# Performance work log

Measured on AMD Instinct MI355X. Metric: run time of the kernel, lower is better.

Reference implementation:

```python
import jax, jax.numpy as jnp
import numpy as np

N_NODES = 100000
N_EDGES = 1250000
IN_CH = 128
OUT_CH = 64


def setup_inputs() -> dict:
    key = jax.random.key(0)
    k1, k2, k3, k4 = jax.random.split(key, 4)
    x = jax.random.normal(k1, (N_NODES, IN_CH), dtype=jnp.float32)
    edge_index = jax.random.randint(k2, (2, N_EDGES), 0, N_NODES, dtype=jnp.int64)
    edge_weight = jax.random.uniform(k3, (N_EDGES,), dtype=jnp.float32)
    # Xavier-uniform weight, zero bias (as in reset_parameters)
    limit = float(np.sqrt(6.0 / (IN_CH + OUT_CH)))
    W = jax.random.uniform(k4, (IN_CH, OUT_CH), dtype=jnp.float32, minval=-limit, maxval=limit)
    b = jnp.zeros((OUT_CH,), dtype=jnp.float32)
    return {"x": x, "edge_index": edge_index, "edge_weight": edge_weight, "W": W, "b": b}


def reference(x, edge_index, edge_weight, W, b):
    # Dense transform: [N, in] @ [in, out] -> [N, out]
    h = jnp.matmul(x, W)
    row, col = edge_index[0], edge_index[1]
    n = h.shape[0]
    # Weighted in-degree via scatter-add on destination (row)
    deg = jnp.zeros((n,), dtype=h.dtype).at[row].add(edge_weight)
    # deg^-0.5 with inf (deg==0) replaced by 0
    deg_inv_sqrt = jnp.where(deg == 0, jnp.zeros_like(deg), deg ** -0.5)
    norm = deg_inv_sqrt[row] * deg_inv_sqrt[col]  # [E]
    # Gather source features, normalize, scatter-add to destinations
    out = jnp.zeros_like(h).at[row].add(h[col] * norm[:, None])
    return out + b
```

## Files before the change

kernel.cpp:

```cpp
#include <hip/hip_runtime.h>

#define N_NODES 100000
#define N_EDGES 1250000
#define IN_CH 128
#define OUT_CH 64

#define BIN_NODES 256
#define NBINS 391
#define BINCAP_DEF 4096
#define NB1 256
#define B1T 512
#define CH1 ((N_EDGES + NB1 - 1) / NB1)
#define MAXU ((CH1 + B1T - 1) / B1T)
#define CURS_STRIDE 16

typedef __attribute__((ext_vector_type(8))) short short8;
typedef __attribute__((ext_vector_type(4))) float f32x4;

__device__ inline unsigned int f2bf(float f) {
    unsigned int u = __float_as_uint(f);
    unsigned int r = ((u >> 16) & 1u) + 0x7FFFu;
    return (u + r) >> 16;
}
__device__ inline float bf_lo(unsigned int p) { return __uint_as_float(p << 16); }
__device__ inline float bf_hi(unsigned int p) { return __uint_as_float(p & 0xFFFF0000u); }

__global__ __launch_bounds__(256) void wbconv_kernel(const float* __restrict__ W,
                                                     unsigned int* __restrict__ Wb,
                                                     int* __restrict__ cursor,
                                                     int bincap) {
    int g = blockIdx.x * 256 + threadIdx.x;
    if (g < NBINS) cursor[g * CURS_STRIDE] = g * bincap;

    int c = g >> 8;
    int t = (g >> 6) & 3;
    int l = g & 63;
    int q = l >> 4, r15 = l & 15;
    unsigned int o[4];
#pragma unroll
    for (int jj = 0; jj < 4; ++jj) {
        float f0 = W[(c * 32 + q * 8 + 2 * jj)     * OUT_CH + t * 16 + r15];
        float f1 = W[(c * 32 + q * 8 + 2 * jj + 1) * OUT_CH + t * 16 + r15];
        o[jj] = f2bf(f0) | (f2bf(f1) << 16);
    }
    *(uint4*)(Wb + (size_t)g * 4) = make_uint4(o[0], o[1], o[2], o[3]);
}

__global__ __launch_bounds__(B1T) void bin1_kernel(const int* __restrict__ ei,
                                                   const float* __restrict__ ew,
                                                   int* __restrict__ cursor,
                                                   int2* __restrict__ brec,
                                                   int bincap) {
    __shared__ int hist[NBINS];
    __shared__ int base[NBINS];
    __shared__ int rank[NBINS];
    const int t = threadIdx.x;
    for (int i = t; i < NBINS; i += B1T) { hist[i] = 0; rank[i] = 0; }
    __syncthreads();

    const int e0 = blockIdx.x * CH1;
    const int e1 = (e0 + CH1 < N_EDGES) ? e0 + CH1 : N_EDGES;

    int rowv[MAXU], colv[MAXU];
    float wv[MAXU];
#pragma unroll
    for (int u = 0; u < MAXU; ++u) {
        int e = e0 + t + u * B1T;
        bool ok = e < e1;
        rowv[u] = ok ? ei[e] : -1;
        colv[u] = ok ? ei[N_EDGES + e] : 0;
        wv[u]   = ok ? ew[e] : 0.0f;
        if (ok) atomicAdd(&hist[rowv[u] >> 8], 1);
    }
    __syncthreads();

    for (int i = t; i < NBINS; i += B1T)
        if (hist[i] > 0) base[i] = atomicAdd(&cursor[i * CURS_STRIDE], hist[i]);
    __syncthreads();

#pragma unroll
    for (int u = 0; u < MAXU; ++u) {
        if (rowv[u] >= 0) {
            int b = rowv[u] >> 8;
            int rk = atomicAdd(&rank[b], 1);
            int idx = base[b] + rk;
            if (idx < (b + 1) * bincap)
                brec[idx] = make_int2(((rowv[u] & 255) << 17) | colv[u],
                                      __float_as_int(wv[u]));
        }
    }
}

__global__ __launch_bounds__(256) void bin2_kernel(const int* __restrict__ cursor,
                                                   const int2* __restrict__ brec,
                                                   int* __restrict__ srt,
                                                   int* __restrict__ cnt_g,
                                                   int* __restrict__ start_g,
                                                   float* __restrict__ dis_g,
                                                   int bincap) {
    __shared__ int   cnt[256];
    __shared__ int   scan[256];
    __shared__ int   slot[256];
    __shared__ float deg[256];
    __shared__ int   wsum[4];
    const int t = threadIdx.x;
    const int b = blockIdx.x;
    cnt[t] = 0; slot[t] = 0; deg[t] = 0.0f;
    __syncthreads();

    const int rbase = b * bincap;
    int m = cursor[b * CURS_STRIDE] - rbase;
    if (m > bincap) m = bincap;

    for (int j = t; j < m; j += 256) {
        int2 rec = brec[rbase + j];
        int rl = rec.x >> 17;
        atomicAdd(&cnt[rl], 1);
        atomicAdd(&deg[rl], __int_as_float(rec.y));
    }
    __syncthreads();

    int v = cnt[t];
    int x = v;
    int lane = t & 63;
#pragma unroll
    for (int off = 1; off < 64; off <<= 1) {
        int y = __shfl_up(x, off, 64);
        if (lane >= off) x += y;
    }
    if (lane == 63) wsum[t >> 6] = x;
    __syncthreads();
    int wbase = 0;
#pragma unroll
    for (int k = 0; k < 4; ++k)
        if (k < (t >> 6)) wbase += wsum[k];
    int mystart = wbase + x - v;

    int node = b * BIN_NODES + t;
    if (node < N_NODES) {
        cnt_g[node]   = v;
        start_g[node] = rbase + mystart;
        float d = deg[t];
        dis_g[node] = (d == 0.0f) ? 0.0f : (1.0f / sqrtf(d));
    }
    scan[t] = mystart;
    __syncthreads();

    for (int j = t; j < m; j += 256) {
        int2 rec = brec[rbase + j];
        int rl  = rec.x >> 17;
        int col = rec.x & 0x1FFFF;
        int sc = atomicAdd(&slot[rl], 1);
        srt[rbase + scan[rl] + sc] = col;
    }
}

__global__ __launch_bounds__(256) void gemm_kernel(const float* __restrict__ x,
                                                   const unsigned int* __restrict__ Wb,
                                                   const float* __restrict__ dis,
                                                   unsigned int* __restrict__ hs) {
    const int tid  = threadIdx.x;
    const int w    = tid >> 6;
    const int lane = tid & 63;
    const int q    = lane >> 4, r15 = lane & 15;
    const int node = blockIdx.x * 64 + w * 16 + r15;
    const int nl   = (node < N_NODES) ? node : N_NODES - 1;
    const float* xrow = x + (size_t)nl * IN_CH;

    f32x4 acc[4];
#pragma unroll
    for (int t = 0; t < 4; ++t) acc[t] = (f32x4){0.f, 0.f, 0.f, 0.f};

#pragma unroll
    for (int c = 0; c < 4; ++c) {
        float4 xa = *(const float4*)(xrow + c * 32 + q * 8);
        float4 xb = *(const float4*)(xrow + c * 32 + q * 8 + 4);
        short8 bfrag;
        bfrag[0] = (short)f2bf(xa.x); bfrag[1] = (short)f2bf(xa.y);
        bfrag[2] = (short)f2bf(xa.z); bfrag[3] = (short)f2bf(xa.w);
        bfrag[4] = (short)f2bf(xb.x); bfrag[5] = (short)f2bf(xb.y);
        bfrag[6] = (short)f2bf(xb.z); bfrag[7] = (short)f2bf(xb.w);
#pragma unroll
        for (int t = 0; t < 4; ++t) {
            short8 afrag = *(const short8*)(Wb + (size_t)((c * 4 + t) * 64 + lane) * 4);
            acc[t] = __builtin_amdgcn_mfma_f32_16x16x32_bf16(afrag, bfrag, acc[t], 0, 0, 0);
        }
    }

    if (node < N_NODES) {
        float di = dis[node];
#pragma unroll
        for (int t = 0; t < 4; ++t) {
            unsigned int p0 = f2bf(acc[t][0] * di) | (f2bf(acc[t][1] * di) << 16);
            unsigned int p1 = f2bf(acc[t][2] * di) | (f2bf(acc[t][3] * di) << 16);
            *(uint2*)(hs + (size_t)node * 32 + t * 8 + q * 2) = make_uint2(p0, p1);
        }
    }
}

__global__ __launch_bounds__(256) void gather_kernel(const int* __restrict__ start,
                                                     const int* __restrict__ cnt,
                                                     const int* __restrict__ srt,
                                                     const float* __restrict__ dis,
                                                     const uint4* __restrict__ hs,
                                                     const float* __restrict__ b,
                                                     float* __restrict__ out) {
    int lane = threadIdx.x & 63;
    int sub  = lane >> 3;
    int l    = lane & 7;
    int i = (blockIdx.x * 4 + (threadIdx.x >> 6)) * 8 + sub;
    if (i >= N_NODES) return;

    int s = start[i];
    int n = cnt[i];
    float a0 = 0.f, a1 = 0.f, a2 = 0.f, a3 = 0.f;
    float a4 = 0.f, a5 = 0.f, a6 = 0.f, a7 = 0.f;
    int j = 0;
    for (; j + 1 < n; j += 2) {
        int c0 = srt[s + j];
        int c1 = srt[s + j + 1];
        uint4 p0 = hs[(size_t)c0 * 8 + l];
        uint4 p1 = hs[(size_t)c1 * 8 + l];
        a0 += bf_lo(p0.x); a1 += bf_hi(p0.x); a2 += bf_lo(p0.y); a3 += bf_hi(p0.y);
        a4 += bf_lo(p0.z); a5 += bf_hi(p0.z); a6 += bf_lo(p0.w); a7 += bf_hi(p0.w);
        a0 += bf_lo(p1.x); a1 += bf_hi(p1.x); a2 += bf_lo(p1.y); a3 += bf_hi(p1.y);
        a4 += bf_lo(p1.z); a5 += bf_hi(p1.z); a6 += bf_lo(p1.w); a7 += bf_hi(p1.w);
    }
    if (j < n) {
        int c0 = srt[s + j];
        uint4 p0 = hs[(size_t)c0 * 8 + l];
        a0 += bf_lo(p0.x); a1 += bf_hi(p0.x); a2 += bf_lo(p0.y); a3 += bf_hi(p0.y);
        a4 += bf_lo(p0.z); a5 += bf_hi(p0.z); a6 += bf_lo(p0.w); a7 += bf_hi(p0.w);
    }
    float di = dis[i];
    float4 b0 = *(const float4*)&b[8 * l];
    float4 b1 = *(const float4*)&b[8 * l + 4];
    float4 o0 = make_float4(a0 * di + b0.x, a1 * di + b0.y, a2 * di + b0.z, a3 * di + b0.w);
    float4 o1 = make_float4(a4 * di + b1.x, a5 * di + b1.y, a6 * di + b1.z, a7 * di + b1.w);
    *(float4*)&out[(size_t)i * OUT_CH + 8 * l]     = o0;
    *(float4*)&out[(size_t)i * OUT_CH + 8 * l + 4] = o1;
}

extern "C" void kernel_launch(void* const* d_in, const int* in_sizes, int n_in,
                              void* d_out, int out_size, void* d_ws, size_t ws_size,
                              hipStream_t stream) {
    const float* x  = (const float*)d_in[0];
    const int*   ei = (const int*)d_in[1];
    const float* ew = (const float*)d_in[2];
    const float* W  = (const float*)d_in[3];
    const float* b  = (const float*)d_in[4];
    float* out = (float*)d_out;

    unsigned int* hs = (unsigned int*)d_ws;
    unsigned int* Wb = hs + (size_t)N_NODES * 32;
    int*   cursor  = (int*)(Wb + 4096);
    int*   cnt_g   = cursor + NBINS * CURS_STRIDE;
    int*   start_g = cnt_g + N_NODES;
    float* dis     = (float*)(start_g + N_NODES);
    int2*  brec    = (int2*)(dis + N_NODES);
    size_t used = (size_t)N_NODES * 32 + 4096 + (size_t)NBINS * CURS_STRIDE
                + 3 * (size_t)N_NODES;
    size_t rem  = (ws_size / 4 > used) ? ws_size / 4 - used : 0;
    int bincap  = (int)(rem / (3 * (size_t)NBINS));
    if (bincap > BINCAP_DEF) bincap = BINCAP_DEF;
    int* srt = (int*)(brec + (size_t)NBINS * bincap);

    wbconv_kernel<<<4, 256, 0, stream>>>(W, Wb, cursor, bincap);
    bin1_kernel<<<NB1, B1T, 0, stream>>>(ei, ew, cursor, brec, bincap);
    bin2_kernel<<<NBINS, 256, 0, stream>>>(cursor, brec, srt, cnt_g, start_g, dis, bincap);
    gemm_kernel<<<(N_NODES + 63) / 64, 256, 0, stream>>>(x, Wb, dis, hs);
    gather_kernel<<<(N_NODES + 31) / 32, 256, 0, stream>>>(start_g, cnt_g, srt, dis,
                                                           (const uint4*)hs, b, out);
}
```

Baseline: 172.4 us.

## Replace CSR sort and gather with per-bin LDS atomic accumulation

```diff
diff --git a/kernel.cpp b/kernel.cpp
--- a/kernel.cpp
+++ b/kernel.cpp
@@ -5,8 +5,9 @@
 #define IN_CH 128
 #define OUT_CH 64
 
-#define BIN_NODES 256
-#define NBINS 391
+#define NPB 224
+#define ACCS 65
+#define NBINS 447
 #define BINCAP_DEF 4096
 #define NB1 256
 #define B1T 512
@@ -16,6 +17,10 @@
 
 typedef __attribute__((ext_vector_type(8))) short short8;
 typedef __attribute__((ext_vector_type(4))) float f32x4;
+
+__device__ __host__ inline int bin_of(int row) {
+    return (int)((unsigned)((row >> 5) * 9363) >> 16);
+}
 
 __device__ inline unsigned int f2bf(float f) {
     unsigned int u = __float_as_uint(f);
@@ -70,7 +75,7 @@
         rowv[u] = ok ? ei[e] : -1;
         colv[u] = ok ? ei[N_EDGES + e] : 0;
         wv[u]   = ok ? ew[e] : 0.0f;
-        if (ok) atomicAdd(&hist[rowv[u] >> 8], 1);
+        if (ok) atomicAdd(&hist[bin_of(rowv[u])], 1);
     }
     __syncthreads();
 
@@ -81,11 +86,11 @@
 #pragma unroll
     for (int u = 0; u < MAXU; ++u) {
         if (rowv[u] >= 0) {
-            int b = rowv[u] >> 8;
+            int b = bin_of(rowv[u]);
             int rk = atomicAdd(&rank[b], 1);
             int idx = base[b] + rk;
             if (idx < (b + 1) * bincap)
-                brec[idx] = make_int2(((rowv[u] & 255) << 17) | colv[u],
+                brec[idx] = make_int2(((rowv[u] - b * NPB) << 17) | colv[u],
                                       __float_as_int(wv[u]));
         }
     }
@@ -93,19 +98,12 @@
 
 __global__ __launch_bounds__(256) void bin2_kernel(const int* __restrict__ cursor,
                                                    const int2* __restrict__ brec,
-                                                   int* __restrict__ srt,
-                                                   int* __restrict__ cnt_g,
-                                                   int* __restrict__ start_g,
                                                    float* __restrict__ dis_g,
                                                    int bincap) {
-    __shared__ int   cnt[256];
-    __shared__ int   scan[256];
-    __shared__ int   slot[256];
-    __shared__ float deg[256];
-    __shared__ int   wsum[4];
+    __shared__ float deg[NPB];
     const int t = threadIdx.x;
     const int b = blockIdx.x;
-    cnt[t] = 0; slot[t] = 0; deg[t] = 0.0f;
+    if (t < NPB) deg[t] = 0.0f;
     __syncthreads();
 
     const int rbase = b * bincap;
@@ -114,44 +112,14 @@
 
     for (int j = t; j < m; j += 256) {
         int2 rec = brec[rbase + j];
-        int rl = rec.x >> 17;
-        atomicAdd(&cnt[rl], 1);
-        atomicAdd(&deg[rl], __int_as_float(rec.y));
-    }
-    __syncthreads();
-
-    int v = cnt[t];
-    int x = v;
-    int lane = t & 63;
-#pragma unroll
-    for (int off = 1; off < 64; off <<= 1) {
-        int y = __shfl_up(x, off, 64);
-        if (lane >= off) x += y;
-    }
-    if (lane == 63) wsum[t >> 6] = x;
-    __syncthreads();
-    int wbase = 0;
-#pragma unroll
-    for (int k = 0; k < 4; ++k)
-        if (k < (t >> 6)) wbase += wsum[k];
-    int mystart = wbase + x - v;
-
-    int node = b * BIN_NODES + t;
-    if (node < N_NODES) {
-        cnt_g[node]   = v;
-        start_g[node] = rbase + mystart;
+        atomicAdd(&deg[rec.x >> 17], __int_as_float(rec.y));
+    }
+    __syncthreads();
+
+    int node = b * NPB + t;
+    if (t < NPB && node < N_NODES) {
         float d = deg[t];
         dis_g[node] = (d == 0.0f) ? 0.0f : (1.0f / sqrtf(d));
-    }
-    scan[t] = mystart;
-    __syncthreads();
-
-    for (int j = t; j < m; j += 256) {
-        int2 rec = brec[rbase + j];
-        int rl  = rec.x >> 17;
-        int col = rec.x & 0x1FFFF;
-        int sc = atomicAdd(&slot[rl], 1);
-        srt[rbase + scan[rl] + sc] = col;
     }
 }
 
@@ -198,47 +166,62 @@
     }
 }
 
-__global__ __launch_bounds__(256) void gather_kernel(const int* __restrict__ start,
-                                                     const int* __restrict__ cnt,
-                                                     const int* __restrict__ srt,
-                                                     const float* __restrict__ dis,
-                                                     const uint4* __restrict__ hs,
-                                                     const float* __restrict__ b,
-                                                     float* __restrict__ out) {
-    int lane = threadIdx.x & 63;
-    int sub  = lane >> 3;
-    int l    = lane & 7;
-    int i = (blockIdx.x * 4 + (threadIdx.x >> 6)) * 8 + sub;
-    if (i >= N_NODES) return;
-
-    int s = start[i];
-    int n = cnt[i];
-    float a0 = 0.f, a1 = 0.f, a2 = 0.f, a3 = 0.f;
-    float a4 = 0.f, a5 = 0.f, a6 = 0.f, a7 = 0.f;
-    int j = 0;
-    for (; j + 1 < n; j += 2) {
-        int c0 = srt[s + j];
-        int c1 = srt[s + j + 1];
-        uint4 p0 = hs[(size_t)c0 * 8 + l];
-        uint4 p1 = hs[(size_t)c1 * 8 + l];
-        a0 += bf_lo(p0.x); a1 += bf_hi(p0.x); a2 += bf_lo(p0.y); a3 += bf_hi(p0.y);
-        a4 += bf_lo(p0.z); a5 += bf_hi(p0.z); a6 += bf_lo(p0.w); a7 += bf_hi(p0.w);
-        a0 += bf_lo(p1.x); a1 += bf_hi(p1.x); a2 += bf_lo(p1.y); a3 += bf_hi(p1.y);
-        a4 += bf_lo(p1.z); a5 += bf_hi(p1.z); a6 += bf_lo(p1.w); a7 += bf_hi(p1.w);
-    }
-    if (j < n) {
-        int c0 = srt[s + j];
-        uint4 p0 = hs[(size_t)c0 * 8 + l];
-        a0 += bf_lo(p0.x); a1 += bf_hi(p0.x); a2 += bf_lo(p0.y); a3 += bf_hi(p0.y);
-        a4 += bf_lo(p0.z); a5 += bf_hi(p0.z); a6 += bf_lo(p0.w); a7 += bf_hi(p0.w);
-    }
-    float di = dis[i];
-    float4 b0 = *(const float4*)&b[8 * l];
-    float4 b1 = *(const float4*)&b[8 * l + 4];
-    float4 o0 = make_float4(a0 * di + b0.x, a1 * di + b0.y, a2 * di + b0.z, a3 * di + b0.w);
-    float4 o1 = make_float4(a4 * di + b1.x, a5 * di + b1.y, a6 * di + b1.z, a7 * di + b1.w);
-    *(float4*)&out[(size_t)i * OUT_CH + 8 * l]     = o0;
-    *(float4*)&out[(size_t)i * OUT_CH + 8 * l + 4] = o1;
+__global__ __launch_bounds__(256) void bingather_kernel(const int* __restrict__ cursor,
+                                                        const int2* __restrict__ brec,
+                                                        const uint4* __restrict__ hs,
+                                                        const float* __restrict__ dis,
+                                                        const float* __restrict__ b,
+                                                        float* __restrict__ out,
+                                                        int bincap) {
+    __shared__ float acc[NPB * ACCS];
+    const int t = threadIdx.x;
+    const int blk = blockIdx.x;
+    for (int k = t; k < NPB * ACCS; k += 256) acc[k] = 0.0f;
+    __syncthreads();
+
+    const int rbase = blk * bincap;
+    int m = cursor[blk * CURS_STRIDE] - rbase;
+    if (m > bincap) m = bincap;
+
+    const int wid = t >> 6, lane = t & 63;
+    const int sub = lane >> 3, l8 = lane & 7;
+
+    for (int j0 = wid * 16; j0 < m; j0 += 64) {
+        int jA = j0 + sub;
+        int jB = j0 + 8 + sub;
+        bool okA = jA < m, okB = jB < m;
+        int recA = okA ? brec[rbase + jA].x : 0;
+        int recB = okB ? brec[rbase + jB].x : 0;
+        uint4 pA, pB;
+        if (okA) pA = hs[(size_t)(recA & 0x1FFFF) * 8 + l8];
+        if (okB) pB = hs[(size_t)(recB & 0x1FFFF) * 8 + l8];
+        if (okA) {
+            float* a = &acc[(recA >> 17) * ACCS + 8 * l8];
+            atomicAdd(a + 0, bf_lo(pA.x)); atomicAdd(a + 1, bf_hi(pA.x));
+            atomicAdd(a + 2, bf_lo(pA.y)); atomicAdd(a + 3, bf_hi(pA.y));
+            atomicAdd(a + 4, bf_lo(pA.z)); atomicAdd(a + 5, bf_hi(pA.z));
+            atomicAdd(a + 6, bf_lo(pA.w)); atomicAdd(a + 7, bf_hi(pA.w));
+        }
+        if (okB) {
+            float* a = &acc[(recB >> 17) * ACCS + 8 * l8];
+            atomicAdd(a + 0, bf_lo(pB.x)); atomicAdd(a + 1, bf_hi(pB.x));
+            atomicAdd(a + 2, bf_lo(pB.y)); atomicAdd(a + 3, bf_hi(pB.y));
+            atomicAdd(a + 4, bf_lo(pB.z)); atomicAdd(a + 5, bf_hi(pB.z));
+            atomicAdd(a + 6, bf_lo(pB.w)); atomicAdd(a + 7, bf_hi(pB.w));
+        }
+    }
+    __syncthreads();
+
+    float bc = b[lane];
+#pragma unroll 4
+    for (int r = 0; r < 56; ++r) {
+        int nl = wid * 56 + r;
+        int node = blk * NPB + nl;
+        if (node < N_NODES) {
+            float di = dis[node];
+            out[(size_t)node * OUT_CH + lane] = acc[nl * ACCS + lane] * di + bc;
+        }
+    }
 }
 
 extern "C" void kernel_launch(void* const* d_in, const int* in_sizes, int n_in,
@@ -254,21 +237,18 @@
     unsigned int* hs = (unsigned int*)d_ws;
     unsigned int* Wb = hs + (size_t)N_NODES * 32;
     int*   cursor  = (int*)(Wb + 4096);
-    int*   cnt_g   = cursor + NBINS * CURS_STRIDE;
-    int*   start_g = cnt_g + N_NODES;
-    float* dis     = (float*)(start_g + N_NODES);
+    float* dis     = (float*)(cursor + NBINS * CURS_STRIDE);
     int2*  brec    = (int2*)(dis + N_NODES);
     size_t used = (size_t)N_NODES * 32 + 4096 + (size_t)NBINS * CURS_STRIDE
-                + 3 * (size_t)N_NODES;
+                + (size_t)N_NODES;
     size_t rem  = (ws_size / 4 > used) ? ws_size / 4 - used : 0;
-    int bincap  = (int)(rem / (3 * (size_t)NBINS));
+    int bincap  = (int)(rem / (2 * (size_t)NBINS));
     if (bincap > BINCAP_DEF) bincap = BINCAP_DEF;
-    int* srt = (int*)(brec + (size_t)NBINS * bincap);
 
     wbconv_kernel<<<4, 256, 0, stream>>>(W, Wb, cursor, bincap);
     bin1_kernel<<<NB1, B1T, 0, stream>>>(ei, ew, cursor, brec, bincap);
-    bin2_kernel<<<NBINS, 256, 0, stream>>>(cursor, brec, srt, cnt_g, start_g, dis, bincap);
+    bin2_kernel<<<NBINS, 256, 0, stream>>>(cursor, brec, dis, bincap);
     gemm_kernel<<<(N_NODES + 63) / 64, 256, 0, stream>>>(x, Wb, dis, hs);
-    gather_kernel<<<(N_NODES + 31) / 32, 256, 0, stream>>>(start_g, cnt_g, srt, dis,
-                                                           (const uint4*)hs, b, out);
-}
+    bingather_kernel<<<NBINS, 256, 0, stream>>>(cursor, brec, (const uint4*)hs,
+                                                dis, b, out, bincap);
+}
```

Measured after the change: 614.2 us. +256.3%, slower.
